# Performance work log

Hardware: AMD Instinct MI355X
Metric: run time of the kernel (lower is better)

The kernel has to match this reference:

```python
import jax, jax.numpy as jnp
import numpy as np

B, S, D, H = 2, 2048, 1024, 16
HD = D // H
NEG = -10000000000.0

def setup_inputs() -> dict:
    key = jax.random.key(0)
    ks = jax.random.split(key, 9)
    s = 1.0 / np.sqrt(D)
    return {
        "x": jax.random.normal(ks[0], (B, S, D), dtype=jnp.float32),
        "Wq": jax.random.uniform(ks[1], (D, D), jnp.float32, -s, s),
        "bq": jax.random.uniform(ks[2], (D,), jnp.float32, -s, s),
        "Wk": jax.random.uniform(ks[3], (D, D), jnp.float32, -s, s),
        "bk": jax.random.uniform(ks[4], (D,), jnp.float32, -s, s),
        "Wv": jax.random.uniform(ks[5], (D, D), jnp.float32, -s, s),
        "bv": jax.random.uniform(ks[6], (D,), jnp.float32, -s, s),
        "Wo": jax.random.uniform(ks[7], (D, D), jnp.float32, -s, s),
        "bo": jax.random.uniform(ks[8], (D,), jnp.float32, -s, s),
    }

def reference(x, Wq, bq, Wk, bk, Wv, bv, Wo, bo):
    b, s, _ = x.shape
    def split_heads(t):
        return t.reshape(b, s, H, HD).transpose(0, 2, 1, 3)  # [b,h,s,hd]
    Q = split_heads(x @ Wq + bq)
    K = split_heads(x @ Wk + bk)
    V = split_heads(x @ Wv + bv)
    scores = jnp.einsum('bhqd,bhkd->bhqk', Q, K) / jnp.sqrt(jnp.float32(HD))
    causal = jnp.tril(jnp.ones((s, s), dtype=bool))
    scores = jnp.where(causal[None, None], scores, NEG)
    attn = jax.nn.softmax(scores, axis=-1)
    ctx = jnp.einsum('bhqk,bhkd->bhqd', attn, V)
    ctx = ctx.transpose(0, 2, 1, 3).reshape(b, s, D)
    return ctx @ Wo + bo
```

## Files before the change

kernel.cpp:

```cpp
#include <hip/hip_runtime.h>
#include <hip/hip_bf16.h>

#define BB 2
#define SS 2048
#define DD 1024
#define HH 16
#define HD 64
#define MM (BB*SS)

typedef __attribute__((ext_vector_type(8))) short bf16x8;
typedef __attribute__((ext_vector_type(4))) float f32x4;
typedef __attribute__((ext_vector_type(16))) float f32x16;

#define QSCALE 0.18033688f

static __device__ __forceinline__ unsigned short f2bf(float f) {
    unsigned int u = __builtin_bit_cast(unsigned int, f);
    u += 0x7fffu + ((u >> 16) & 1u);
    return (unsigned short)(u >> 16);
}

static __device__ __forceinline__ void gload16(const unsigned short* g, unsigned short* l) {
    __builtin_amdgcn_global_load_lds(
        (const __attribute__((address_space(1))) unsigned int*)g,
        (__attribute__((address_space(3))) unsigned int*)l, 16, 0, 0);
}

__global__ __launch_bounds__(256) void prep_kernel(const float* __restrict__ x,
                                                   const float* __restrict__ W0,
                                                   const float* __restrict__ W1,
                                                   const float* __restrict__ W2,
                                                   const float* __restrict__ W3,
                                                   unsigned short* __restrict__ xb,
                                                   unsigned short* __restrict__ Wt)
{
    const int t = threadIdx.x;
    const int bid = blockIdx.x;
    if (bid < 2048) {
        const size_t i = ((size_t)bid * 256 + t) * 8;
        float4 a = *(const float4*)(x + i);
        float4 b = *(const float4*)(x + i + 4);
        union { unsigned short u[8]; bf16x8 v; } pk;
        pk.u[0] = f2bf(a.x); pk.u[1] = f2bf(a.y); pk.u[2] = f2bf(a.z); pk.u[3] = f2bf(a.w);
        pk.u[4] = f2bf(b.x); pk.u[5] = f2bf(b.y); pk.u[6] = f2bf(b.z); pk.u[7] = f2bf(b.w);
        *(bf16x8*)(xb + i) = pk.v;
        return;
    }
    __shared__ unsigned short Ts[64][72];
    const int wsel = (bid - 2048) >> 8;
    const int rem  = (bid - 2048) & 255;
    const float* W = wsel == 0 ? W0 : wsel == 1 ? W1 : wsel == 2 ? W2 : W3;
    unsigned short* out = Wt + (size_t)wsel * DD * DD;
    const int n0 = (rem & 15) * 64, k0 = (rem >> 4) * 64;
#pragma unroll
    for (int i = 0; i < 4; ++i) {
        const int r = (t >> 4) + i * 16;
        const int c = (t & 15) * 4;
        float4 v = *(const float4*)(W + (size_t)(k0 + r) * DD + n0 + c);
        Ts[c + 0][r] = f2bf(v.x); Ts[c + 1][r] = f2bf(v.y);
        Ts[c + 2][r] = f2bf(v.z); Ts[c + 3][r] = f2bf(v.w);
    }
    __syncthreads();
#pragma unroll
    for (int j = 0; j < 2; ++j) {
        const int ch = j * 256 + t;
        const int rn = ch >> 3, ck = (ch & 7) * 8;
        bf16x8 v = *(const bf16x8*)&Ts[rn][ck];
        *(bf16x8*)(out + (size_t)(n0 + rn) * DD + k0 + ck) = v;
    }
}

__global__ __launch_bounds__(256) void gemm_mfma(const unsigned short* __restrict__ A,
                                                 const unsigned short* __restrict__ Bt,
                                                 const float* __restrict__ bias0,
                                                 const float* __restrict__ bias1,
                                                 const float* __restrict__ bias2,
                                                 unsigned short* __restrict__ Qb,
                                                 unsigned short* __restrict__ Kb,
                                                 unsigned short* __restrict__ Vb,
                                                 float* __restrict__ outf,
                                                 int mode)
{
    __shared__ unsigned short As[2][128 * 64];
    __shared__ unsigned short Bs[2][128 * 64];

    const int t = threadIdx.x;
    const int w = t >> 6, l = t & 63;
    const int lane16 = l & 15, quad = l >> 4;
    const int m0 = blockIdx.x * 128, n0 = blockIdx.y * 128;
    const int wm = (w & 1) * 64, wn = (w >> 1) * 64;

    f32x4 acc[4][4] = {};

    int srow[4], skcg[4];
#pragma unroll
    for (int j = 0; j < 4; ++j) {
        const int c = t + j * 256;
        srow[j] = c >> 3;
        skcg[j] = (c & 7) ^ (srow[j] & 7);
    }

#pragma unroll
    for (int j = 0; j < 4; ++j) {
        const int c = t + j * 256;
        gload16(A  + (size_t)(m0 + srow[j]) * DD + skcg[j] * 8, &As[0][c * 8]);
        gload16(Bt + (size_t)(n0 + srow[j]) * DD + skcg[j] * 8, &Bs[0][c * 8]);
    }
    __syncthreads();

#pragma unroll 2
    for (int kt = 0; kt < 16; ++kt) {
        const int cur = kt & 1;
        if (kt + 1 < 16) {
            const int k1 = (kt + 1) * 64;
#pragma unroll
            for (int j = 0; j < 4; ++j) {
                const int c = t + j * 256;
                gload16(A  + (size_t)(m0 + srow[j]) * DD + k1 + skcg[j] * 8, &As[cur ^ 1][c * 8]);
                gload16(Bt + (size_t)(n0 + srow[j]) * DD + k1 + skcg[j] * 8, &Bs[cur ^ 1][c * 8]);
            }
        }
#pragma unroll
        for (int h = 0; h < 2; ++h) {
            bf16x8 af[4], bfr[4];
#pragma unroll
            for (int mt = 0; mt < 4; ++mt) {
                const int row = wm + mt * 16 + lane16;
                af[mt] = *(const bf16x8*)&As[cur][(row * 8 + ((h * 4 + quad) ^ (row & 7))) * 8];
            }
#pragma unroll
            for (int nt = 0; nt < 4; ++nt) {
                const int row = wn + nt * 16 + lane16;
                bfr[nt] = *(const bf16x8*)&Bs[cur][(row * 8 + ((h * 4 + quad) ^ (row & 7))) * 8];
            }
#pragma unroll
            for (int mt = 0; mt < 4; ++mt)
#pragma unroll
                for (int nt = 0; nt < 4; ++nt)
                    acc[mt][nt] = __builtin_amdgcn_mfma_f32_16x16x32_bf16(af[mt], bfr[nt], acc[mt][nt], 0, 0, 0);
        }
        __syncthreads();
    }

    if (mode == 0) {
        const int which = n0 >> 10;
        const float* bias = which == 0 ? bias0 : which == 1 ? bias1 : bias2;
#pragma unroll
        for (int nt = 0; nt < 4; ++nt) {
            const int gcol = n0 + wn + nt * 16 + lane16;
            const int cd = gcol & 1023;
            const float bv = bias[cd];
            const int h_ = cd >> 6, d = cd & 63;
            if (which == 2) {
#pragma unroll
                for (int mt = 0; mt < 4; ++mt) {
                    const int row0 = m0 + wm + mt * 16 + quad * 4;
                    const int b_ = row0 >> 11, s0 = row0 & 2047;
                    union { unsigned short u[4]; uint2 v; } pk;
#pragma unroll
                    for (int r = 0; r < 4; ++r) pk.u[r] = f2bf(acc[mt][nt][r] + bv);
                    *(uint2*)(Vb + ((size_t)(b_ * HH + h_) * HD + d) * SS + s0) = pk.v;
                }
            } else {
                unsigned short* dst3 = which == 0 ? Qb : Kb;
                const float sc_ = which == 0 ? QSCALE : 1.0f;
#pragma unroll
                for (int mt = 0; mt < 4; ++mt)
#pragma unroll
                    for (int r = 0; r < 4; ++r) {
                        const int row = m0 + wm + mt * 16 + quad * 4 + r;
                        const int b_ = row >> 11, s_ = row & 2047;
                        dst3[(((size_t)(b_ * HH + h_) * SS + s_) * HD) + d] =
                            f2bf((acc[mt][nt][r] + bv) * sc_);
                    }
            }
        }
    } else {
#pragma unroll
        for (int nt = 0; nt < 4; ++nt) {
            const int gcol = n0 + wn + nt * 16 + lane16;
            const float bv = bias0[gcol];
#pragma unroll
            for (int mt = 0; mt < 4; ++mt)
#pragma unroll
                for (int r = 0; r < 4; ++r) {
                    const int row = m0 + wm + mt * 16 + quad * 4 + r;
                    outf[(size_t)row * DD + gcol] = acc[mt][nt][r] + bv;
                }
        }
    }
}

__global__ __launch_bounds__(512) void attn_mfma(const unsigned short* __restrict__ Q,
                                                 const unsigned short* __restrict__ K,
                                                 const unsigned short* __restrict__ V,
                                                 unsigned short* __restrict__ ctx)
{
    __shared__ unsigned short Ks[4][4096];
    __shared__ unsigned short Vs[4][4096];

    const int t = threadIdx.x;
    const int w = t >> 6, l = t & 63;
    const int l31 = l & 31, hi = l >> 5;
    const int qg = w & 3, par = w >> 2;
    const int bid = blockIdx.x;
    const int halfg = bid >> 8, idx = bid & 255;
    const int qb_ = idx >> 5;
    const int qblk = halfg ? qb_ : 15 - qb_;
    const int hb = idx & 31;
    const int h = hb & 15, b = hb >> 4;
    const int q0 = qblk * 128;
    const size_t bh = (size_t)(b * HH + h) * SS;
    const unsigned short* Vg = V + (size_t)(b * HH + h) * HD * SS;

    const int wq0 = q0 + qg * 32;
    bf16x8 qf[4];
#pragma unroll
    for (int dt = 0; dt < 4; ++dt)
        qf[dt] = *(const bf16x8*)(Q + (bh + wq0 + l31) * HD + dt * 16 + hi * 8);

    f32x16 ot[2] = {};
    float lp = 0.f;

    const int ntiles = 2 * qblk + 2;
    const int sr = t >> 3;
    const int sg = (t & 7) ^ (sr & 7);

    {
        uint4 ka  = *(const uint4*)(K + (bh + sr) * HD + sg * 8);
        uint4 kb2 = *(const uint4*)(K + (bh + 64 + sr) * HD + sg * 8);
        uint4 va  = *(const uint4*)(Vg + (size_t)sr * SS + sg * 8);
        uint4 vb2 = *(const uint4*)(Vg + (size_t)sr * SS + 64 + sg * 8);
        *(uint4*)&Ks[0][t * 8] = ka;
        *(uint4*)&Ks[1][t * 8] = kb2;
        *(uint4*)&Vs[0][t * 8] = va;
        *(uint4*)&Vs[1][t * 8] = vb2;
    }
    asm volatile("s_waitcnt lgkmcnt(0)" ::: "memory");
    __builtin_amdgcn_sched_barrier(0);
    __builtin_amdgcn_s_barrier();

    const int nsup = ntiles >> 1;
    for (int st = 0; st < nsup; ++st) {
        uint4 ka, kb2, va, vb2;
        const bool pre = (2 * st + 2 < ntiles);
        if (pre) {
            const int kaof = (2 * st + 2) * 64, kbof = kaof + 64;
            ka  = *(const uint4*)(K + (bh + kaof + sr) * HD + sg * 8);
            kb2 = *(const uint4*)(K + (bh + kbof + sr) * HD + sg * 8);
            va  = *(const uint4*)(Vg + (size_t)sr * SS + kaof + sg * 8);
            vb2 = *(const uint4*)(Vg + (size_t)sr * SS + kbof + sg * 8);
        }
        __builtin_amdgcn_sched_barrier(0);

        const int mt = 2 * st + par;
        const int k0 = mt * 64;
        if (k0 <= wq0 + 31) {
            const unsigned short* Kt = Ks[mt & 3];
            const unsigned short* Vt = Vs[mt & 3];

            f32x16 s[2] = {};
            __builtin_amdgcn_s_setprio(1);
#pragma unroll
            for (int dt = 0; dt < 4; ++dt) {
#pragma unroll
                for (int kh = 0; kh < 2; ++kh) {
                    const int row = kh * 32 + l31;
                    bf16x8 kf = *(const bf16x8*)&Kt[(row * 8 + ((dt * 2 + hi) ^ (row & 7))) * 8];
                    s[kh] = __builtin_amdgcn_mfma_f32_32x32x16_bf16(kf, qf[dt], s[kh], 0, 0, 0);
                }
            }
            __builtin_amdgcn_s_setprio(0);

            if (k0 + 63 > wq0) {
                const int q = wq0 + l31;
#pragma unroll
                for (int kh = 0; kh < 2; ++kh)
#pragma unroll
                    for (int r = 0; r < 16; ++r) {
                        const int k = k0 + kh * 32 + (r & 3) + 8 * (r >> 2) + 4 * hi;
                        if (k > q) s[kh][r] = -1e30f;
                    }
            }

#pragma unroll
            for (int kh = 0; kh < 2; ++kh) {
#pragma unroll
                for (int r = 0; r < 16; ++r) s[kh][r] = __builtin_amdgcn_exp2f(s[kh][r]);
                const float t0 = (s[kh][0] + s[kh][1]) + (s[kh][2] + s[kh][3]);
                const float t1 = (s[kh][4] + s[kh][5]) + (s[kh][6] + s[kh][7]);
                const float t2 = (s[kh][8] + s[kh][9]) + (s[kh][10] + s[kh][11]);
                const float t3 = (s[kh][12] + s[kh][13]) + (s[kh][14] + s[kh][15]);
                lp += (t0 + t1) + (t2 + t3);
            }

#pragma unroll
            for (int kh = 0; kh < 2; ++kh) {
#pragma unroll
                for (int c = 0; c < 2; ++c) {
                    const int rb = c * 8;
                    unsigned int w0, w1, w2, w3;
                    asm("v_cvt_pk_bf16_f32 %0, %1, %2" : "=v"(w0) : "v"(s[kh][rb + 0]), "v"(s[kh][rb + 1]));
                    asm("v_cvt_pk_bf16_f32 %0, %1, %2" : "=v"(w2) : "v"(s[kh][rb + 4]), "v"(s[kh][rb + 5]));
                    asm("v_cvt_pk_bf16_f32 %0, %1, %2" : "=v"(w1) : "v"(s[kh][rb + 2]), "v"(s[kh][rb + 3]));
                    asm("v_cvt_pk_bf16_f32 %0, %1, %2" : "=v"(w3) : "v"(s[kh][rb + 6]), "v"(s[kh][rb + 7]));
                    asm("v_permlane32_swap_b32 %0, %1" : "+v"(w0), "+v"(w2));
                    asm("v_permlane32_swap_b32 %0, %1" : "+v"(w1), "+v"(w3));
                    union { unsigned int u[4]; bf16x8 v; } pa;
                    pa.u[0] = w0; pa.u[1] = w1; pa.u[2] = w2; pa.u[3] = w3;
                    const int chunk = kh * 4 + c * 2 + hi;
                    const int rlo = l31, rhi2 = 32 + l31;
                    bf16x8 v0 = *(const bf16x8*)&Vt[(rlo * 8 + (chunk ^ (rlo & 7))) * 8];
                    bf16x8 v1 = *(const bf16x8*)&Vt[(rhi2 * 8 + (chunk ^ (rhi2 & 7))) * 8];
                    __builtin_amdgcn_s_setprio(1);
                    ot[0] = __builtin_amdgcn_mfma_f32_32x32x16_bf16(v0, pa.v, ot[0], 0, 0, 0);
                    ot[1] = __builtin_amdgcn_mfma_f32_32x32x16_bf16(v1, pa.v, ot[1], 0, 0, 0);
                    __builtin_amdgcn_s_setprio(0);
                }
            }
        }

        if (pre) {
            const int ba = (2 * st + 2) & 3, bb3 = (2 * st + 3) & 3;
            *(uint4*)&Ks[ba][t * 8] = ka;
            *(uint4*)&Ks[bb3][t * 8] = kb2;
            *(uint4*)&Vs[ba][t * 8] = va;
            *(uint4*)&Vs[bb3][t * 8] = vb2;
        }
        asm volatile("s_waitcnt lgkmcnt(0)" ::: "memory");
        __builtin_amdgcn_sched_barrier(0);
        __builtin_amdgcn_s_barrier();
    }

    float* Osh = (float*)&Ks[0][0];
    float* Lsh = (float*)&Vs[0][0];
    if (par == 1) {
#pragma unroll
        for (int a2 = 0; a2 < 2; ++a2)
#pragma unroll
            for (int r = 0; r < 16; ++r) Osh[qg * 2048 + (a2 * 16 + r) * 64 + l] = ot[a2][r];
        Lsh[qg * 64 + l] = lp;
    }
    __syncthreads();
    if (par == 0) {
#pragma unroll
        for (int a2 = 0; a2 < 2; ++a2)
#pragma unroll
            for (int r = 0; r < 16; ++r) ot[a2][r] += Osh[qg * 2048 + (a2 * 16 + r) * 64 + l];
        lp += Lsh[qg * 64 + l];

        lp += __shfl_xor(lp, 32);
        const float inv = 1.f / lp;

        const int qrow = wq0 + l31;
        unsigned short* dst = ctx + ((size_t)(b * SS) + qrow) * DD + h * HD;
#pragma unroll
        for (int a2 = 0; a2 < 2; ++a2)
#pragma unroll
            for (int u = 0; u < 4; ++u) {
                const int d0 = a2 * 32 + 8 * u + 4 * hi;
                union { unsigned short u4[4]; uint2 v; } pk;
#pragma unroll
                for (int r = 0; r < 4; ++r) pk.u4[r] = f2bf(ot[a2][4 * u + r] * inv);
                *(uint2*)(dst + d0) = pk.v;
            }
    }
}

extern "C" void kernel_launch(void* const* d_in, const int* in_sizes, int n_in,
                              void* d_out, int out_size, void* d_ws, size_t ws_size,
                              hipStream_t stream) {
    const float* x  = (const float*)d_in[0];
    const float* Wq = (const float*)d_in[1];
    const float* bq = (const float*)d_in[2];
    const float* Wk = (const float*)d_in[3];
    const float* bk = (const float*)d_in[4];
    const float* Wv = (const float*)d_in[5];
    const float* bv = (const float*)d_in[6];
    const float* Wo = (const float*)d_in[7];
    const float* bo = (const float*)d_in[8];
    float* out = (float*)d_out;

    unsigned short* xb  = (unsigned short*)d_ws;
    unsigned short* Wt  = xb  + (size_t)MM * DD;
    unsigned short* Qb  = Wt  + (size_t)4 * DD * DD;
    unsigned short* Kb  = Qb  + (size_t)MM * DD;
    unsigned short* Vb  = Kb  + (size_t)MM * DD;
    unsigned short* ctxb = Vb + (size_t)MM * DD;

    prep_kernel<<<2048 + 1024, 256, 0, stream>>>(x, Wq, Wk, Wv, Wo, xb, Wt);

    gemm_mfma<<<dim3(MM / 128, 3072 / 128), 256, 0, stream>>>(
        xb, Wt, bq, bk, bv, Qb, Kb, Vb, nullptr, 0);

    attn_mfma<<<(SS / 128) * HH * BB, 512, 0, stream>>>(Qb, Kb, Vb, ctxb);

    gemm_mfma<<<dim3(MM / 128, DD / 128), 256, 0, stream>>>(
        ctxb, Wt + (size_t)3 * DD * DD, bo, nullptr, nullptr,
        nullptr, nullptr, nullptr, out, 1);
}
```

Baseline: 184.5 us.

## Deepen GEMM LDS pipeline to four K=32 stages with prefetch distance two

Restructures the projection GEMM main loop from a double-buffered K=64 tile to a four-slot ring of K=32 tiles, issuing global-to-LDS loads two iterations ahead. It uses explicit vmcnt waits and raw s_barrier in place of __syncthreads, so the wait covers only the oldest outstanding stage. The XOR swizzle is adapted to the 4-chunk row layout. The aim is to hide global load latency better. In exchange there are more barriers per K and less MFMA work per iteration, and correctness relies on the hand-written wait counts.

```diff
diff --git a/kernel.cpp b/kernel.cpp
--- a/kernel.cpp
+++ b/kernel.cpp
@@ -81,8 +81,8 @@
                                                  float* __restrict__ outf,
                                                  int mode)
 {
-    __shared__ unsigned short As[2][128 * 64];
-    __shared__ unsigned short Bs[2][128 * 64];
+    __shared__ unsigned short As[4][128 * 32];
+    __shared__ unsigned short Bs[4][128 * 32];
 
     const int t = threadIdx.x;
     const int w = t >> 6, l = t & 63;
@@ -92,55 +92,66 @@
 
     f32x4 acc[4][4] = {};
 
-    int srow[4], skcg[4];
-#pragma unroll
-    for (int j = 0; j < 4; ++j) {
+    int srow[2], sgc[2];
+#pragma unroll
+    for (int j = 0; j < 2; ++j) {
         const int c = t + j * 256;
-        srow[j] = c >> 3;
-        skcg[j] = (c & 7) ^ (srow[j] & 7);
-    }
-
-#pragma unroll
-    for (int j = 0; j < 4; ++j) {
-        const int c = t + j * 256;
-        gload16(A  + (size_t)(m0 + srow[j]) * DD + skcg[j] * 8, &As[0][c * 8]);
-        gload16(Bt + (size_t)(n0 + srow[j]) * DD + skcg[j] * 8, &Bs[0][c * 8]);
-    }
-    __syncthreads();
+        srow[j] = c >> 2;
+        sgc[j] = (c & 3) ^ ((srow[j] >> 1) & 3);
+    }
+
+#define STAGE(ktile)                                                                   \
+    {                                                                                  \
+        const int k1_ = (ktile) * 32;                                                  \
+        const int bi_ = (ktile) & 3;                                                   \
+        _Pragma("unroll")                                                              \
+        for (int j = 0; j < 2; ++j) {                                                  \
+            gload16(A  + (size_t)(m0 + srow[j]) * DD + k1_ + sgc[j] * 8,               \
+                    &As[bi_][(t + j * 256) * 8]);                                      \
+            gload16(Bt + (size_t)(n0 + srow[j]) * DD + k1_ + sgc[j] * 8,               \
+                    &Bs[bi_][(t + j * 256) * 8]);                                      \
+        }                                                                              \
+    }
+
+    STAGE(0);
+    STAGE(1);
+    asm volatile("s_waitcnt vmcnt(4)" ::: "memory");
+    __builtin_amdgcn_sched_barrier(0);
+    __builtin_amdgcn_s_barrier();
 
 #pragma unroll 2
-    for (int kt = 0; kt < 16; ++kt) {
-        const int cur = kt & 1;
-        if (kt + 1 < 16) {
-            const int k1 = (kt + 1) * 64;
-#pragma unroll
-            for (int j = 0; j < 4; ++j) {
-                const int c = t + j * 256;
-                gload16(A  + (size_t)(m0 + srow[j]) * DD + k1 + skcg[j] * 8, &As[cur ^ 1][c * 8]);
-                gload16(Bt + (size_t)(n0 + srow[j]) * DD + k1 + skcg[j] * 8, &Bs[cur ^ 1][c * 8]);
-            }
-        }
-#pragma unroll
-        for (int h = 0; h < 2; ++h) {
-            bf16x8 af[4], bfr[4];
-#pragma unroll
-            for (int mt = 0; mt < 4; ++mt) {
-                const int row = wm + mt * 16 + lane16;
-                af[mt] = *(const bf16x8*)&As[cur][(row * 8 + ((h * 4 + quad) ^ (row & 7))) * 8];
-            }
-#pragma unroll
-            for (int nt = 0; nt < 4; ++nt) {
-                const int row = wn + nt * 16 + lane16;
-                bfr[nt] = *(const bf16x8*)&Bs[cur][(row * 8 + ((h * 4 + quad) ^ (row & 7))) * 8];
-            }
-#pragma unroll
-            for (int mt = 0; mt < 4; ++mt)
-#pragma unroll
-                for (int nt = 0; nt < 4; ++nt)
-                    acc[mt][nt] = __builtin_amdgcn_mfma_f32_16x16x32_bf16(af[mt], bfr[nt], acc[mt][nt], 0, 0, 0);
-        }
-        __syncthreads();
-    }
+    for (int kt = 0; kt < 32; ++kt) {
+        if (kt + 2 < 32) STAGE(kt + 2);
+
+        const unsigned short* Ab = As[kt & 3];
+        const unsigned short* Bb = Bs[kt & 3];
+        bf16x8 af[4], bfr[4];
+#pragma unroll
+        for (int mt = 0; mt < 4; ++mt) {
+            const int row = wm + mt * 16 + lane16;
+            af[mt] = *(const bf16x8*)&Ab[(row * 4 + (quad ^ ((row >> 1) & 3))) * 8];
+        }
+#pragma unroll
+        for (int nt = 0; nt < 4; ++nt) {
+            const int row = wn + nt * 16 + lane16;
+            bfr[nt] = *(const bf16x8*)&Bb[(row * 4 + (quad ^ ((row >> 1) & 3))) * 8];
+        }
+#pragma unroll
+        for (int mt = 0; mt < 4; ++mt)
+#pragma unroll
+            for (int nt = 0; nt < 4; ++nt)
+                acc[mt][nt] = __builtin_amdgcn_mfma_f32_16x16x32_bf16(af[mt], bfr[nt], acc[mt][nt], 0, 0, 0);
+
+        __builtin_amdgcn_sched_barrier(0);
+        if (kt + 2 < 32) {
+            asm volatile("s_waitcnt vmcnt(4)" ::: "memory");
+        } else {
+            asm volatile("s_waitcnt vmcnt(0)" ::: "memory");
+        }
+        __builtin_amdgcn_sched_barrier(0);
+        __builtin_amdgcn_s_barrier();
+    }
+#undef STAGE
 
     if (mode == 0) {
         const int which = n0 >> 10;
```

New measurement: 197.3 us. 6.9% more time.

## Compute softmax row sums via MFMA with ones and shrink output GEMM tile

Applied to the files above, without the earlier changes.

In attention, the per-row sum of exponentiated scores is now accumulated by an extra MFMA against a vector of bf16 ones, replacing the scalar adds and the final cross-lane shuffle. This moves VALU work onto the matrix units, at the cost of one more MFMA per P·V step and a sum taken over bf16-rounded probabilities. The GEMM is templated on M tile size, and the output projection uses 64-row tiles so it launches twice as many blocks and fills the GPU better, with less reuse of each B tile.

```diff
diff --git a/kernel.cpp b/kernel.cpp
--- a/kernel.cpp
+++ b/kernel.cpp
@@ -70,6 +70,7 @@
     }
 }
 
+template<int BM>
 __global__ __launch_bounds__(256) void gemm_mfma(const unsigned short* __restrict__ A,
                                                  const unsigned short* __restrict__ Bt,
                                                  const float* __restrict__ bias0,
@@ -81,17 +82,27 @@
                                                  float* __restrict__ outf,
                                                  int mode)
 {
-    __shared__ unsigned short As[2][128 * 64];
+    constexpr int MT = BM / 32;
+    constexpr int NA = BM / 32;
+
+    __shared__ unsigned short As[2][BM * 64];
     __shared__ unsigned short Bs[2][128 * 64];
 
     const int t = threadIdx.x;
     const int w = t >> 6, l = t & 63;
     const int lane16 = l & 15, quad = l >> 4;
-    const int m0 = blockIdx.x * 128, n0 = blockIdx.y * 128;
-    const int wm = (w & 1) * 64, wn = (w >> 1) * 64;
-
-    f32x4 acc[4][4] = {};
-
+    const int m0 = blockIdx.x * BM, n0 = blockIdx.y * 128;
+    const int wm = (w & 1) * (BM / 2), wn = (w >> 1) * 64;
+
+    f32x4 acc[MT][4] = {};
+
+    int arow[NA], akcg[NA];
+#pragma unroll
+    for (int j = 0; j < NA; ++j) {
+        const int c = t + j * 256;
+        arow[j] = c >> 3;
+        akcg[j] = (c & 7) ^ (arow[j] & 7);
+    }
     int srow[4], skcg[4];
 #pragma unroll
     for (int j = 0; j < 4; ++j) {
@@ -101,11 +112,11 @@
     }
 
 #pragma unroll
-    for (int j = 0; j < 4; ++j) {
-        const int c = t + j * 256;
-        gload16(A  + (size_t)(m0 + srow[j]) * DD + skcg[j] * 8, &As[0][c * 8]);
-        gload16(Bt + (size_t)(n0 + srow[j]) * DD + skcg[j] * 8, &Bs[0][c * 8]);
-    }
+    for (int j = 0; j < NA; ++j)
+        gload16(A + (size_t)(m0 + arow[j]) * DD + akcg[j] * 8, &As[0][(t + j * 256) * 8]);
+#pragma unroll
+    for (int j = 0; j < 4; ++j)
+        gload16(Bt + (size_t)(n0 + srow[j]) * DD + skcg[j] * 8, &Bs[0][(t + j * 256) * 8]);
     __syncthreads();
 
 #pragma unroll 2
@@ -114,17 +125,17 @@
         if (kt + 1 < 16) {
             const int k1 = (kt + 1) * 64;
 #pragma unroll
-            for (int j = 0; j < 4; ++j) {
-                const int c = t + j * 256;
-                gload16(A  + (size_t)(m0 + srow[j]) * DD + k1 + skcg[j] * 8, &As[cur ^ 1][c * 8]);
-                gload16(Bt + (size_t)(n0 + srow[j]) * DD + k1 + skcg[j] * 8, &Bs[cur ^ 1][c * 8]);
-            }
+            for (int j = 0; j < NA; ++j)
+                gload16(A + (size_t)(m0 + arow[j]) * DD + k1 + akcg[j] * 8, &As[cur ^ 1][(t + j * 256) * 8]);
+#pragma unroll
+            for (int j = 0; j < 4; ++j)
+                gload16(Bt + (size_t)(n0 + srow[j]) * DD + k1 + skcg[j] * 8, &Bs[cur ^ 1][(t + j * 256) * 8]);
         }
 #pragma unroll
         for (int h = 0; h < 2; ++h) {
-            bf16x8 af[4], bfr[4];
-#pragma unroll
-            for (int mt = 0; mt < 4; ++mt) {
+            bf16x8 af[MT], bfr[4];
+#pragma unroll
+            for (int mt = 0; mt < MT; ++mt) {
                 const int row = wm + mt * 16 + lane16;
                 af[mt] = *(const bf16x8*)&As[cur][(row * 8 + ((h * 4 + quad) ^ (row & 7))) * 8];
             }
@@ -134,7 +145,7 @@
                 bfr[nt] = *(const bf16x8*)&Bs[cur][(row * 8 + ((h * 4 + quad) ^ (row & 7))) * 8];
             }
 #pragma unroll
-            for (int mt = 0; mt < 4; ++mt)
+            for (int mt = 0; mt < MT; ++mt)
 #pragma unroll
                 for (int nt = 0; nt < 4; ++nt)
                     acc[mt][nt] = __builtin_amdgcn_mfma_f32_16x16x32_bf16(af[mt], bfr[nt], acc[mt][nt], 0, 0, 0);
@@ -153,7 +164,7 @@
             const int h_ = cd >> 6, d = cd & 63;
             if (which == 2) {
 #pragma unroll
-                for (int mt = 0; mt < 4; ++mt) {
+                for (int mt = 0; mt < MT; ++mt) {
                     const int row0 = m0 + wm + mt * 16 + quad * 4;
                     const int b_ = row0 >> 11, s0 = row0 & 2047;
                     union { unsigned short u[4]; uint2 v; } pk;
@@ -165,7 +176,7 @@
                 unsigned short* dst3 = which == 0 ? Qb : Kb;
                 const float sc_ = which == 0 ? QSCALE : 1.0f;
 #pragma unroll
-                for (int mt = 0; mt < 4; ++mt)
+                for (int mt = 0; mt < MT; ++mt)
 #pragma unroll
                     for (int r = 0; r < 4; ++r) {
                         const int row = m0 + wm + mt * 16 + quad * 4 + r;
@@ -181,7 +192,7 @@
             const int gcol = n0 + wn + nt * 16 + lane16;
             const float bv = bias0[gcol];
 #pragma unroll
-            for (int mt = 0; mt < 4; ++mt)
+            for (int mt = 0; mt < MT; ++mt)
 #pragma unroll
                 for (int r = 0; r < 4; ++r) {
                     const int row = m0 + wm + mt * 16 + quad * 4 + r;
@@ -219,8 +230,12 @@
     for (int dt = 0; dt < 4; ++dt)
         qf[dt] = *(const bf16x8*)(Q + (bh + wq0 + l31) * HD + dt * 16 + hi * 8);
 
+    bf16x8 ones;
+#pragma unroll
+    for (int i = 0; i < 8; ++i) ones[i] = (short)0x3F80;
+
     f32x16 ot[2] = {};
-    float lp = 0.f;
+    f32x16 lacc = {};
 
     const int ntiles = 2 * qblk + 2;
     const int sr = t >> 3;
@@ -284,15 +299,9 @@
             }
 
 #pragma unroll
-            for (int kh = 0; kh < 2; ++kh) {
+            for (int kh = 0; kh < 2; ++kh)
 #pragma unroll
                 for (int r = 0; r < 16; ++r) s[kh][r] = __builtin_amdgcn_exp2f(s[kh][r]);
-                const float t0 = (s[kh][0] + s[kh][1]) + (s[kh][2] + s[kh][3]);
-                const float t1 = (s[kh][4] + s[kh][5]) + (s[kh][6] + s[kh][7]);
-                const float t2 = (s[kh][8] + s[kh][9]) + (s[kh][10] + s[kh][11]);
-                const float t3 = (s[kh][12] + s[kh][13]) + (s[kh][14] + s[kh][15]);
-                lp += (t0 + t1) + (t2 + t3);
-            }
 
 #pragma unroll
             for (int kh = 0; kh < 2; ++kh) {
@@ -315,6 +324,7 @@
                     __builtin_amdgcn_s_setprio(1);
                     ot[0] = __builtin_amdgcn_mfma_f32_32x32x16_bf16(v0, pa.v, ot[0], 0, 0, 0);
                     ot[1] = __builtin_amdgcn_mfma_f32_32x32x16_bf16(v1, pa.v, ot[1], 0, 0, 0);
+                    lacc  = __builtin_amdgcn_mfma_f32_32x32x16_bf16(ones, pa.v, lacc, 0, 0, 0);
                     __builtin_amdgcn_s_setprio(0);
                 }
             }
@@ -332,6 +342,8 @@
         __builtin_amdgcn_s_barrier();
     }
 
+    float lp = lacc[0];
+
     float* Osh = (float*)&Ks[0][0];
     float* Lsh = (float*)&Vs[0][0];
     if (par == 1) {
@@ -349,7 +361,6 @@
             for (int r = 0; r < 16; ++r) ot[a2][r] += Osh[qg * 2048 + (a2 * 16 + r) * 64 + l];
         lp += Lsh[qg * 64 + l];
 
-        lp += __shfl_xor(lp, 32);
         const float inv = 1.f / lp;
 
         const int qrow = wq0 + l31;
@@ -390,12 +401,12 @@
 
     prep_kernel<<<2048 + 1024, 256, 0, stream>>>(x, Wq, Wk, Wv, Wo, xb, Wt);
 
-    gemm_mfma<<<dim3(MM / 128, 3072 / 128), 256, 0, stream>>>(
+    gemm_mfma<128><<<dim3(MM / 128, 3072 / 128), 256, 0, stream>>>(
         xb, Wt, bq, bk, bv, Qb, Kb, Vb, nullptr, 0);
 
     attn_mfma<<<(SS / 128) * HH * BB, 512, 0, stream>>>(Qb, Kb, Vb, ctxb);
 
-    gemm_mfma<<<dim3(MM / 128, DD / 128), 256, 0, stream>>>(
+    gemm_mfma<64><<<dim3(MM / 64, DD / 128), 256, 0, stream>>>(
         ctxb, Wt + (size_t)3 * DD * DD, bo, nullptr, nullptr,
         nullptr, nullptr, nullptr, out, 1);
 }
```

Result: no change. 182.1 us (median of 2 runs) (-1.3%).
